# Kernel optimization log

Hardware: AMD Instinct MI355X
Metric: run time of the kernel (lower is better)

Reference implementation:

```python
import jax, jax.numpy as jnp
import numpy as np

D_MODEL = 1024
N_HEAD = 16
D_HEAD = 64
BSZ = 2
QLEN = 2048
LOCAL_SIZE = 1000
LN_EPS = 1e-5


def setup_inputs() -> dict:
    key = jax.random.key(0)
    ks = jax.random.split(key, 8)
    z1ss = jax.random.normal(ks[0], (BSZ, D_MODEL, QLEN), jnp.float32)
    pos_emb = jax.random.normal(ks[1], (1, D_MODEL, QLEN), jnp.float32)
    u1ss = jax.random.normal(ks[2], (BSZ, 3 * N_HEAD * D_HEAD, QLEN), jnp.float32) * 0.05
    W_qkv = jax.random.normal(ks[3], (3 * N_HEAD * D_HEAD, D_MODEL), jnp.float32) * 0.02
    W_r = jax.random.normal(ks[4], (N_HEAD * D_HEAD, D_MODEL), jnp.float32) * 0.02
    r_w_bias = jax.random.uniform(ks[5], (N_HEAD, D_HEAD), jnp.float32, -0.05, 0.05)
    r_r_bias = jax.random.uniform(ks[6], (N_HEAD, D_HEAD), jnp.float32, -0.05, 0.05)
    W_o = jax.random.normal(ks[7], (D_MODEL, N_HEAD * D_HEAD), jnp.float32) * 0.02
    b_o = jnp.zeros((D_MODEL,), jnp.float32)
    return dict(z1ss=z1ss, pos_emb=pos_emb, u1ss=u1ss, W_qkv=W_qkv, W_r=W_r,
                r_w_bias=r_w_bias, r_r_bias=r_r_bias, W_o=W_o, b_o=b_o)


def _rel_shift(x):
    # Transformer-XL relative-shift trick: pad one column on the left, reshape,
    # drop first row, reshape back. x: [b, n, qlen, klen]
    b, n, q, k = x.shape
    xp = jnp.pad(x, ((0, 0), (0, 0), (0, 0), (1, 0)))
    return xp.reshape(b, n, k + 1, q)[:, :, 1:, :].reshape(b, n, q, k)


def reference(z1ss, pos_emb, u1ss, W_qkv, W_r, r_w_bias, r_r_bias, W_o, b_o):
    bsz, d_model, qlen = z1ss.shape
    n_head, d_head = r_w_bias.shape
    klen = qlen  # mems=None -> mlen=0
    scale = 1.0 / (d_head ** 0.5)

    # Conv1d(kernel_size=1, bias=False) == per-position linear
    w_heads = jnp.einsum('od,bdq->boq', W_qkv, z1ss) + u1ss        # [b, 3*n*d, q]
    r_head_k = jnp.einsum('od,dq->oq', W_r, pos_emb[0]).reshape(n_head, d_head, klen)

    q_h, k_h, v_h = jnp.split(w_heads, 3, axis=1)
    q_h = q_h.reshape(bsz, n_head, d_head, qlen)
    k_h = k_h.reshape(bsz, n_head, d_head, klen)
    v_h = v_h.reshape(bsz, n_head, d_head, klen)

    AC = jnp.einsum('bndi,bndj->bnij', q_h + r_w_bias[:, :, None], k_h)
    BD = _rel_shift(jnp.einsum('bndi,ndj->bnij', q_h + r_r_bias[:, :, None], r_head_k))
    attn_score = (AC + BD) * scale                                  # [b, n, q, k]

    # causal + local-window mask (mlen=0)
    ones = jnp.ones((qlen, klen), dtype=bool)
    mask = jnp.triu(ones, 1) | jnp.tril(ones, -LOCAL_SIZE)
    attn_score = jnp.where(mask[None, None], -jnp.inf, attn_score)

    attn_prob = jax.nn.softmax(attn_score, axis=-1)
    attn_vec = jnp.einsum('bnij,bndj->bndi', attn_prob, v_h)
    attn_vec = attn_vec.reshape(bsz, n_head * d_head, qlen)

    attn_out = jnp.einsum('od,bdq->boq', W_o, attn_vec) + b_o[None, :, None]

    # post-LN residual: layer_norm over d_model (no affine params)
    x = (attn_out + z1ss).transpose(0, 2, 1)                        # [b, q, d]
    mu = x.mean(-1, keepdims=True)
    var = ((x - mu) ** 2).mean(-1, keepdims=True)
    x = (x - mu) / jnp.sqrt(var + LN_EPS)
    return x.transpose(0, 2, 1)                                     # [b, d, q]
```

## Files before the change

kernel.cpp:

```cpp
#include <hip/hip_runtime.h>
#include <hip/hip_bf16.h>

#define D_MODEL 1024
#define N_HEAD 16
#define BSZ 2
#define QLEN 2048
#define LOCAL_SIZE 1000
#define QKV3 (3 * N_HEAD * 64)

typedef __hip_bfloat16 bf16;
typedef short bf16x8 __attribute__((ext_vector_type(8)));
typedef float f32x4 __attribute__((ext_vector_type(4)));

static __device__ __forceinline__ float b2f(bf16 x) { return __bfloat162float(x); }
static __device__ __forceinline__ float bits2f(unsigned short u) {
    return __uint_as_float(((unsigned int)u) << 16);
}
static __device__ __forceinline__ unsigned short f2bs(float x) {
    __hip_bfloat16 h = __float2bfloat16(x);
    return *(unsigned short*)&h;
}

static __device__ __forceinline__ int rmode(int m, int fl) { return (m == 2) ? fl : m; }
static __device__ __forceinline__ float ldm(const void* p, size_t i, int isf) {
    return isf ? ((const float*)p)[i] : b2f(((const bf16*)p)[i]);
}
static __device__ __forceinline__ float4 ld4(const void* p, size_t i, int isf) {
    if (isf) return ((const float4*)p)[i >> 2];
    ushort4 u = ((const ushort4*)p)[i >> 2];
    float4 f;
    f.x = bits2f(u.x); f.y = bits2f(u.y); f.z = bits2f(u.z); f.w = bits2f(u.w);
    return f;
}
static __device__ __forceinline__ ushort4 cvt4(float4 f) {
    ushort4 u;
    u.x = f2bs(f.x); u.y = f2bs(f.y); u.z = f2bs(f.z); u.w = f2bs(f.w);
    return u;
}

static __device__ __forceinline__ void glds16(const bf16* g, unsigned short* l) {
    __builtin_amdgcn_global_load_lds(
        (const __attribute__((address_space(1))) void*)g,
        (__attribute__((address_space(3))) void*)l,
        16, 0, 0);
}

__global__ void detect_kernel(const unsigned short* __restrict__ w, int* __restrict__ flag)
{
    if (threadIdx.x == 0 && blockIdx.x == 0) {
        int good = 0;
        for (int i = 0; i < 256; ++i) {
            float v = bits2f(w[i]);
            if (v == v && fabsf(v) < 8.0f) ++good;
        }
        *flag = (good >= 240) ? 0 : 1;
    }
}

__global__ __launch_bounds__(256)
void convw_all(const void* __restrict__ wq, const void* __restrict__ wr,
               const void* __restrict__ wo, bf16* __restrict__ outp,
               const int* __restrict__ flag)
{
    const int fl = *flag;
    const int blk = blockIdx.x;
    const void* in; size_t segOff;
    if (blk < 1536)      { in = wq; segOff = (size_t)blk * 2048; }
    else if (blk < 2048) { in = wr; segOff = (size_t)(blk - 1536) * 2048; }
    else                 { in = wo; segOff = (size_t)(blk - 2048) * 2048; }
    const size_t ii = segOff + (size_t)threadIdx.x * 8;
    const size_t oi = (size_t)blk * 2048 + (size_t)threadIdx.x * 8;
    if (fl) {
        float4 a = ((const float4*)in)[ii / 4];
        float4 b = ((const float4*)in)[ii / 4 + 1];
        *(ushort4*)((unsigned short*)outp + oi)     = cvt4(a);
        *(ushort4*)((unsigned short*)outp + oi + 4) = cvt4(b);
    } else {
        *(uint4*)((unsigned short*)outp + oi) = ((const uint4*)in)[ii / 8];
    }
}

__global__ __launch_bounds__(256)
void tcvt_all(const void* __restrict__ z1ss, const void* __restrict__ pos,
              bf16* __restrict__ zt, bf16* __restrict__ post,
              const int* __restrict__ flag)
{
    const int fl = *flag;
    const int zb = blockIdx.z;
    const void* in = (zb < BSZ) ? z1ss : pos;
    const size_t inOff = (zb < BSZ) ? (size_t)zb * D_MODEL * QLEN : 0;
    bf16* outp = (zb < BSZ) ? zt + (size_t)zb * QLEN * D_MODEL : post;
    const int c0 = blockIdx.x * 32;
    const int r0 = blockIdx.y * 32;
    const int tx = threadIdx.x & 31, ty = threadIdx.x >> 5;
    __shared__ float T[32][33];
#pragma unroll
    for (int r = 0; r < 4; ++r) {
        int rr = r0 + ty + r * 8;
        T[ty + r * 8][tx] = ldm(in, inOff + (size_t)rr * QLEN + c0 + tx, fl);
    }
    __syncthreads();
#pragma unroll
    for (int r = 0; r < 4; ++r) {
        int cc = c0 + ty + r * 8;
        outp[(size_t)cc * D_MODEL + r0 + tx] = __float2bfloat16(T[tx][ty + r * 8]);
    }
}

__global__ __launch_bounds__(256)
void gemm_qkvr(const bf16* __restrict__ wqb, const bf16* __restrict__ wrb,
               const bf16* __restrict__ zt, const bf16* __restrict__ post,
               bf16* __restrict__ wh, bf16* __restrict__ rhk,
               const void* __restrict__ u1ss, const int* __restrict__ flag)
{
    const int fl = *flag;
    const int bz = blockIdx.z;
    const int by = blockIdx.y;
    const bool isR = by >= (QKV3 / 128);
    if (isR && bz) return;
    const int n0 = blockIdx.x * 128;
    const int m0 = (isR ? by - QKV3 / 128 : by) * 128;
    const int K = D_MODEL, N = QLEN;

    const bf16* A = isR ? wrb : wqb;
    const bf16* B = isR ? post : zt + (size_t)bz * (size_t)QLEN * D_MODEL;
    bf16* C       = isR ? rhk  : wh + (size_t)bz * (size_t)QKV3 * QLEN;
    const size_t uOff = (size_t)bz * (size_t)QKV3 * QLEN;

    const int tid = threadIdx.x;
    const int wave = tid >> 6, lane = tid & 63;
    const int quad = lane >> 4, l15 = lane & 15;
    const int wm = (wave >> 1) * 64, wn = (wave & 1) * 64;

    __shared__ __align__(16) unsigned short A_s[2][128 * 32];
    __shared__ __align__(16) unsigned short B_s[2][128 * 32];

    const int srow = wave * 32 + (lane >> 2);
    const int scol = (lane & 3) * 8;
    const bf16* Ag = A + (size_t)(m0 + srow) * K + scol;
    const bf16* Bg = B + (size_t)(n0 + srow) * K + scol;
    const int sbase = wave * 1024;

    f32x4 acc[4][4];
#pragma unroll
    for (int i = 0; i < 4; ++i)
#pragma unroll
        for (int j = 0; j < 4; ++j) acc[i][j] = (f32x4){0.f, 0.f, 0.f, 0.f};

    glds16(Ag,                   &A_s[0][sbase]);
    glds16(Ag + (size_t)16 * K,  &A_s[0][sbase + 512]);
    glds16(Bg,                   &B_s[0][sbase]);
    glds16(Bg + (size_t)16 * K,  &B_s[0][sbase + 512]);

    int cur = 0;
    for (int k0 = 0; k0 < K; k0 += 32) {
        __syncthreads();
        if (k0 + 32 < K) {
            const int kn = k0 + 32;
            glds16(Ag + kn,                  &A_s[cur ^ 1][sbase]);
            glds16(Ag + (size_t)16 * K + kn, &A_s[cur ^ 1][sbase + 512]);
            glds16(Bg + kn,                  &B_s[cur ^ 1][sbase]);
            glds16(Bg + (size_t)16 * K + kn, &B_s[cur ^ 1][sbase + 512]);
        }
        bf16x8 a[4], bb[4];
#pragma unroll
        for (int i = 0; i < 4; ++i)
            a[i] = *(const bf16x8*)&A_s[cur][(wm + i * 16 + l15) * 32 + quad * 8];
#pragma unroll
        for (int j = 0; j < 4; ++j)
            bb[j] = *(const bf16x8*)&B_s[cur][(wn + j * 16 + l15) * 32 + quad * 8];
#pragma unroll
        for (int i = 0; i < 4; ++i)
#pragma unroll
            for (int j = 0; j < 4; ++j)
                acc[i][j] = __builtin_amdgcn_mfma_f32_16x16x32_bf16(a[i], bb[j], acc[i][j], 0, 0, 0);
        cur ^= 1;
    }

#pragma unroll
    for (int i = 0; i < 4; ++i) {
#pragma unroll
        for (int j = 0; j < 4; ++j) {
            int n = n0 + wn + j * 16 + l15;
#pragma unroll
            for (int r = 0; r < 4; ++r) {
                int m = m0 + wm + i * 16 + quad * 4 + r;
                float v = acc[i][j][r];
                if (!isR) v += ldm(u1ss, uOff + (size_t)m * N + n, fl);
                C[(size_t)m * N + n] = __float2bfloat16(v);
            }
        }
    }
}

__global__ __launch_bounds__(256)
void gemm_glds(const bf16* __restrict__ A, size_t sAb,
               const bf16* __restrict__ B, size_t sBb,
               void* __restrict__ C, int c_is_bf16, size_t sCb,
               const void* __restrict__ addm, int mAdd, size_t sAddb,
               const void* __restrict__ bias, int mBias,
               int M, int N, int K, const int* __restrict__ flag)
{
    const int fl = *flag;
    const int fAdd = rmode(mAdd, fl), fBias = rmode(mBias, fl);

    const int bz = blockIdx.z;
    const int n0 = blockIdx.x * 128;
    const int m0 = blockIdx.y * 128;
    const int tid = threadIdx.x;
    const int wave = tid >> 6, lane = tid & 63;
    const int quad = lane >> 4, l15 = lane & 15;
    const int wm = (wave >> 1) * 64, wn = (wave & 1) * 64;

    __shared__ __align__(16) unsigned short A_s[2][128 * 32];
    __shared__ __align__(16) unsigned short B_s[2][128 * 32];

    const int srow = wave * 32 + (lane >> 2);
    const int scol = (lane & 3) * 8;
    const bf16* Ag = A + (size_t)bz * sAb + (size_t)(m0 + srow) * K + scol;
    const bf16* Bg = B + (size_t)bz * sBb + (size_t)(n0 + srow) * K + scol;
    const int sbase = wave * 1024;

    f32x4 acc[4][4];
#pragma unroll
    for (int i = 0; i < 4; ++i)
#pragma unroll
        for (int j = 0; j < 4; ++j) acc[i][j] = (f32x4){0.f, 0.f, 0.f, 0.f};

    glds16(Ag,                   &A_s[0][sbase]);
    glds16(Ag + (size_t)16 * K,  &A_s[0][sbase + 512]);
    glds16(Bg,                   &B_s[0][sbase]);
    glds16(Bg + (size_t)16 * K,  &B_s[0][sbase + 512]);

    int cur = 0;
    for (int k0 = 0; k0 < K; k0 += 32) {
        __syncthreads();
        if (k0 + 32 < K) {
            const int kn = k0 + 32;
            glds16(Ag + kn,                  &A_s[cur ^ 1][sbase]);
            glds16(Ag + (size_t)16 * K + kn, &A_s[cur ^ 1][sbase + 512]);
            glds16(Bg + kn,                  &B_s[cur ^ 1][sbase]);
            glds16(Bg + (size_t)16 * K + kn, &B_s[cur ^ 1][sbase + 512]);
        }
        bf16x8 a[4], bb[4];
#pragma unroll
        for (int i = 0; i < 4; ++i)
            a[i] = *(const bf16x8*)&A_s[cur][(wm + i * 16 + l15) * 32 + quad * 8];
#pragma unroll
        for (int j = 0; j < 4; ++j)
            bb[j] = *(const bf16x8*)&B_s[cur][(wn + j * 16 + l15) * 32 + quad * 8];
#pragma unroll
        for (int i = 0; i < 4; ++i)
#pragma unroll
            for (int j = 0; j < 4; ++j)
                acc[i][j] = __builtin_amdgcn_mfma_f32_16x16x32_bf16(a[i], bb[j], acc[i][j], 0, 0, 0);
        cur ^= 1;
    }

    const size_t cb = (size_t)bz * sCb;
#pragma unroll
    for (int i = 0; i < 4; ++i) {
#pragma unroll
        for (int j = 0; j < 4; ++j) {
            int n = n0 + wn + j * 16 + l15;
#pragma unroll
            for (int r = 0; r < 4; ++r) {
                int m = m0 + wm + i * 16 + quad * 4 + r;
                float v = acc[i][j][r];
                if (addm) v += ldm(addm, (size_t)bz * sAddb + (size_t)m * N + n, fAdd);
                if (bias) v += ldm(bias, (size_t)n, fBias);
                size_t ci = cb + (size_t)m * N + n;
                if (c_is_bf16) ((bf16*)C)[ci] = __float2bfloat16(v);
                else           ((float*)C)[ci] = v;
            }
        }
    }
}

__global__ __launch_bounds__(256)
void gemm_bf16(const void* __restrict__ A, int mA, size_t sAb,
               const void* __restrict__ B, int mB, size_t sBb,
               void* __restrict__ C, int c_is_bf16, size_t sCb,
               const void* __restrict__ addm, int mAdd, size_t sAddb,
               const void* __restrict__ bias, int mBias,
               int M, int N, int K, const int* __restrict__ flag)
{
    const int fl = *flag;
    const int fA = rmode(mA, fl), fB = rmode(mB, fl);
    const int fAdd = rmode(mAdd, fl), fBias = rmode(mBias, fl);

    const int bz = blockIdx.z;
    const int n0 = blockIdx.x * 128;
    const int m0 = blockIdx.y * 128;
    const int tid = threadIdx.x;
    const int wave = tid >> 6, lane = tid & 63;
    const int quad = lane >> 4, l15 = lane & 15;
    const int wm = (wave >> 1) * 64, wn = (wave & 1) * 64;

    __shared__ unsigned short A_s[128][40];
    __shared__ unsigned short B_s[128][40];

    const int r0c = tid >> 2,         c0c = tid & 3;
    const int r1c = (tid + 256) >> 2, c1c = tid & 3;

    const size_t aOff = (size_t)bz * sAb;
    const size_t bOff = (size_t)bz * sBb;
    const bf16*  Ah = (const bf16*)A;
    const float* Af = (const float*)A;
    const bf16*  Bh = (const bf16*)B;
    const float* Bf = (const float*)B;

    uint4 pa[4], pb[4];

#define LOAD_OP(p, fX, Xh, Xf, xOff, R0, C0, R1, C1, base, k0)                          \
    do {                                                                                \
        if (!fX) {                                                                      \
            p[0] = *(const uint4*)(Xh + xOff + (size_t)(base + R0) * K + (k0) + C0 * 8);\
            p[1] = *(const uint4*)(Xh + xOff + (size_t)(base + R1) * K + (k0) + C1 * 8);\
        } else {                                                                        \
            const float* q0 = Xf + xOff + (size_t)(base + R0) * K + (k0) + C0 * 8;      \
            const float* q1 = Xf + xOff + (size_t)(base + R1) * K + (k0) + C1 * 8;      \
            p[0] = *(const uint4*)q0; p[1] = *(const uint4*)(q0 + 4);                   \
            p[2] = *(const uint4*)q1; p[3] = *(const uint4*)(q1 + 4);                   \
        }                                                                               \
    } while (0)

#define WRITE_OP(p, fX, S, R0, C0, R1, C1)                                              \
    do {                                                                                \
        if (!fX) {                                                                      \
            *(uint4*)&S[R0][C0 * 8] = p[0];                                             \
            *(uint4*)&S[R1][C1 * 8] = p[1];                                             \
        } else {                                                                        \
            float4 f0 = *(float4*)&p[0], f1 = *(float4*)&p[1];                          \
            float4 f2 = *(float4*)&p[2], f3 = *(float4*)&p[3];                          \
            *(ushort4*)&S[R0][C0 * 8]     = cvt4(f0);                                   \
            *(ushort4*)&S[R0][C0 * 8 + 4] = cvt4(f1);                                   \
            *(ushort4*)&S[R1][C1 * 8]     = cvt4(f2);                                   \
            *(ushort4*)&S[R1][C1 * 8 + 4] = cvt4(f3);                                   \
        }                                                                               \
    } while (0)

    f32x4 acc[4][4];
#pragma unroll
    for (int i = 0; i < 4; ++i)
#pragma unroll
        for (int j = 0; j < 4; ++j) acc[i][j] = (f32x4){0.f, 0.f, 0.f, 0.f};

    LOAD_OP(pa, fA, Ah, Af, aOff, r0c, c0c, r1c, c1c, m0, 0);
    LOAD_OP(pb, fB, Bh, Bf, bOff, r0c, c0c, r1c, c1c, n0, 0);

    for (int k0 = 0; k0 < K; k0 += 32) {
        WRITE_OP(pa, fA, A_s, r0c, c0c, r1c, c1c);
        WRITE_OP(pb, fB, B_s, r0c, c0c, r1c, c1c);
        __syncthreads();

        const int kn = k0 + 32;
        if (kn < K) {
            LOAD_OP(pa, fA, Ah, Af, aOff, r0c, c0c, r1c, c1c, m0, kn);
            LOAD_OP(pb, fB, Bh, Bf, bOff, r0c, c0c, r1c, c1c, n0, kn);
        }

        bf16x8 a[4], bb[4];
#pragma unroll
        for (int i = 0; i < 4; ++i)
            a[i] = *(const bf16x8*)&A_s[wm + i * 16 + l15][quad * 8];
#pragma unroll
        for (int j = 0; j < 4; ++j)
            bb[j] = *(const bf16x8*)&B_s[wn + j * 16 + l15][quad * 8];
#pragma unroll
        for (int i = 0; i < 4; ++i)
#pragma unroll
            for (int j = 0; j < 4; ++j)
                acc[i][j] = __builtin_amdgcn_mfma_f32_16x16x32_bf16(a[i], bb[j], acc[i][j], 0, 0, 0);
        __syncthreads();
    }
#undef LOAD_OP
#undef WRITE_OP

    const size_t cb = (size_t)bz * sCb;
#pragma unroll
    for (int i = 0; i < 4; ++i) {
#pragma unroll
        for (int j = 0; j < 4; ++j) {
            int n = n0 + wn + j * 16 + l15;
#pragma unroll
            for (int r = 0; r < 4; ++r) {
                int m = m0 + wm + i * 16 + quad * 4 + r;
                float v = acc[i][j][r];
                if (addm) v += ldm(addm, (size_t)bz * sAddb + (size_t)m * N + n, fAdd);
                if (bias) v += ldm(bias, (size_t)n, fBias);
                size_t ci = cb + (size_t)m * N + n;
                if (c_is_bf16) ((bf16*)C)[ci] = __float2bfloat16(v);
                else           ((float*)C)[ci] = v;
            }
        }
    }
}

__global__ __launch_bounds__(256)
void gemm_tn(const void* __restrict__ A, int mA, size_t sAb,
             const void* __restrict__ Bsrc, int mB, int bTrans, int ldB, size_t sBb,
             void* __restrict__ C, int c_is_bf16, size_t sCb,
             const void* __restrict__ addm, int mAdd, int addT, size_t sAddb,
             const void* __restrict__ bias, int mBias,
             int M, int N, int K, const int* __restrict__ flag)
{
    const int fl = *flag;
    const int fA = rmode(mA, fl), fB = rmode(mB, fl);
    const int fAdd = rmode(mAdd, fl), fBias = rmode(mBias, fl);

    const int bz = blockIdx.z;
    const int n0 = blockIdx.x * 128;
    const int m0 = blockIdx.y * 128;
    const int tid = threadIdx.x;
    const int wave = tid >> 6, lane = tid & 63;
    const int quad = lane >> 4, l15 = lane & 15;
    const int wm = (wave >> 1) * 64, wn = (wave & 1) * 64;

    __shared__ unsigned short A_s[128][40];
    __shared__ unsigned short B_s[128][40];

    const size_t aBase = (size_t)bz * sAb;
    const size_t bBase = (size_t)bz * sBb;

    f32x4 acc[4][4];
#pragma unroll
    for (int i = 0; i < 4; ++i)
#pragma unroll
        for (int j = 0; j < 4; ++j) acc[i][j] = (f32x4){0.f, 0.f, 0.f, 0.f};

    for (int k0 = 0; k0 < K; k0 += 32) {
#pragma unroll
        for (int g = 0; g < 4; ++g) {
            int c = tid + g * 256;
            int m = c >> 3, kc = (c & 7) * 4;
            float4 f = ld4(A, aBase + (size_t)(m0 + m) * K + k0 + kc, fA);
            *(ushort4*)&A_s[m][kc] = cvt4(f);
        }
        if (!bTrans) {
#pragma unroll
            for (int g = 0; g < 4; ++g) {
                int c = tid + g * 256;
                int n = c >> 3, kc = (c & 7) * 4;
                float4 f = ld4(Bsrc, bBase + (size_t)(n0 + n) * ldB + k0 + kc, fB);
                *(ushort4*)&B_s[n][kc] = cvt4(f);
            }
        } else {
#pragma unroll
            for (int g = 0; g < 4; ++g) {
                int c = tid + g * 256;
                int k = c >> 5, nc = (c & 31) * 4;
                float4 f = ld4(Bsrc, bBase + (size_t)(k0 + k) * ldB + n0 + nc, fB);
                ushort4 u = cvt4(f);
                B_s[nc + 0][k] = u.x;
                B_s[nc + 1][k] = u.y;
                B_s[nc + 2][k] = u.z;
                B_s[nc + 3][k] = u.w;
            }
        }
        __syncthreads();

        bf16x8 a[4], bb[4];
#pragma unroll
        for (int i = 0; i < 4; ++i)
            a[i] = *(const bf16x8*)&A_s[wm + i * 16 + l15][quad * 8];
#pragma unroll
        for (int j = 0; j < 4; ++j)
            bb[j] = *(const bf16x8*)&B_s[wn + j * 16 + l15][quad * 8];
#pragma unroll
        for (int i = 0; i < 4; ++i)
#pragma unroll
            for (int j = 0; j < 4; ++j)
                acc[i][j] = __builtin_amdgcn_mfma_f32_16x16x32_bf16(a[i], bb[j], acc[i][j], 0, 0, 0);
        __syncthreads();
    }

    const size_t cb = (size_t)bz * sCb;
#pragma unroll
    for (int i = 0; i < 4; ++i) {
#pragma unroll
        for (int j = 0; j < 4; ++j) {
            int n = n0 + wn + j * 16 + l15;
#pragma unroll
            for (int r = 0; r < 4; ++r) {
                int m = m0 + wm + i * 16 + quad * 4 + r;
                float v = acc[i][j][r];
                if (addm) {
                    size_t ai = (size_t)bz * sAddb +
                                (addT ? ((size_t)n * M + m) : ((size_t)m * N + n));
                    v += ldm(addm, ai, fAdd);
                }
                if (bias) v += ldm(bias, (size_t)n, fBias);
                size_t ci = cb + (size_t)m * N + n;
                if (c_is_bf16) ((bf16*)C)[ci] = __float2bfloat16(v);
                else           ((float*)C)[ci] = v;
            }
        }
    }
}

__global__ __launch_bounds__(256)
void attn_mfma(const bf16* __restrict__ wh,
               const bf16* __restrict__ rhk,
               const void* __restrict__ rwb,
               const void* __restrict__ rrb,
               bf16* __restrict__ av_out,
               const int* __restrict__ flag)
{
    const int fl = *flag;
    const int it = blockIdx.x, h = blockIdx.y, b = blockIdx.z;
    const int i0 = it * 64;
    const int tid = threadIdx.x;
    const int wave = tid >> 6, lane = tid & 63;
    const int quad = lane >> 4, l15 = lane & 15;
    const int hw = h * 64;

    __shared__ __align__(16) unsigned short sm[18944];
    unsigned short* KtPs = sm;
    unsigned short* Vs   = sm + 4608;
    unsigned short* Rt   = sm + 9216;
    unsigned short* Gs   = sm + 9216;
    unsigned short* Qrw  = sm;
    unsigned short* Qrr  = sm + 4608;

    const bf16* whb = wh + (size_t)b * QKV3 * QLEN;
    const int d_t = tid & 63;
    const int dv0 = tid >> 3, jv0 = (tid & 7) * 8;
    const int dv1 = (tid + 256) >> 3;

    int lo = i0 - (LOCAL_SIZE - 1);
    if (lo < 0) lo = 0;
    const int jt_lo = lo >> 6;
    const int j0_lo = jt_lo * 64;

    {
        float brw = ldm(rwb, hw + d_t, fl);
        float brr = ldm(rrb, hw + d_t, fl);
        const bf16* qrow = whb + (size_t)(hw + d_t) * QLEN + i0;
        uint4 qv0 = *(const uint4*)(qrow + wave * 8);
        uint4 qv1 = *(const uint4*)(qrow + (4 + wave) * 8);
        const int pbase0 = j0_lo - i0 + QLEN - 64;
        const bf16* rrow = rhk + (size_t)(hw + d_t) * QLEN;
        uint4 rv0i = *(const uint4*)(rrow + pbase0 + wave * 8);
        uint4 rv1i = *(const uint4*)(rrow + pbase0 + (4 + wave) * 8);

        unsigned short u8[8];
        *(uint4*)u8 = qv0;
#pragma unroll
        for (int u = 0; u < 8; ++u) {
            float q = bits2f(u8[u]);
            Qrw[(wave * 8 + u) * 72 + d_t] = f2bs(q + brw);
            Qrr[(wave * 8 + u) * 72 + d_t] = f2bs(q + brr);
        }
        *(uint4*)u8 = qv1;
#pragma unroll
        for (int u = 0; u < 8; ++u) {
            float q = bits2f(u8[u]);
            Qrw[((4 + wave) * 8 + u) * 72 + d_t] = f2bs(q + brw);
            Qrr[((4 + wave) * 8 + u) * 72 + d_t] = f2bs(q + brr);
        }
        *(uint4*)u8 = rv0i;
#pragma unroll
        for (int u = 0; u < 8; ++u) Rt[(wave * 8 + u) * 72 + d_t] = u8[u];
        *(uint4*)u8 = rv1i;
#pragma unroll
        for (int u = 0; u < 8; ++u) Rt[((4 + wave) * 8 + u) * 72 + d_t] = u8[u];
    }

    uint4 kv0, kv1, vv0, vv1, rv0, rv1;
    {
        const int j0 = j0_lo;
        const bf16* krow = whb + (size_t)(1024 + hw + d_t) * QLEN + j0;
        kv0 = *(const uint4*)(krow + wave * 8);
        kv1 = *(const uint4*)(krow + (4 + wave) * 8);
        vv0 = *(const uint4*)(whb + (size_t)(2048 + hw + dv0) * QLEN + j0 + jv0);
        vv1 = *(const uint4*)(whb + (size_t)(2048 + hw + dv1) * QLEN + j0 + jv0);
        const int pn = j0 - i0 + QLEN;
        const bf16* rrow = rhk + (size_t)(hw + d_t) * QLEN;
        int p0 = pn + wave * 8;
        if (p0 + 7 < QLEN) rv0 = *(const uint4*)(rrow + p0);
        else {
            unsigned short u8[8];
#pragma unroll
            for (int u = 0; u < 8; ++u)
                u8[u] = (p0 + u < QLEN) ? *(const unsigned short*)(rrow + p0 + u) : 0;
            rv0 = *(uint4*)u8;
        }
        int p1 = pn + (4 + wave) * 8;
        if (p1 + 7 < QLEN) rv1 = *(const uint4*)(rrow + p1);
        else {
            unsigned short u8[8];
#pragma unroll
            for (int u = 0; u < 8; ++u)
                u8[u] = (p1 + u < QLEN) ? *(const unsigned short*)(rrow + p1 + u) : 0;
            rv1 = *(uint4*)u8;
        }
    }
    __syncthreads();

    const int qrow_off = (wave * 16 + l15) * 72 + quad * 8;
    bf16x8 qw0 = *(const bf16x8*)&Qrw[qrow_off];
    bf16x8 qw1 = *(const bf16x8*)&Qrw[qrow_off + 32];
    bf16x8 qr0 = *(const bf16x8*)&Qrr[qrow_off];
    bf16x8 qr1 = *(const bf16x8*)&Qrr[qrow_off + 32];

    f32x4 g_acc[8];
#pragma unroll
    for (int nt = 0; nt < 4; ++nt) {
        f32x4 g = (f32x4){0.f, 0.f, 0.f, 0.f};
        int ro = (nt * 16 + l15) * 72 + quad * 8;
        bf16x8 b0 = *(const bf16x8*)&Rt[ro];
        bf16x8 b1 = *(const bf16x8*)&Rt[ro + 32];
        g = __builtin_amdgcn_mfma_f32_16x16x32_bf16(qr0, b0, g, 0, 0, 0);
        g = __builtin_amdgcn_mfma_f32_16x16x32_bf16(qr1, b1, g, 0, 0, 0);
        g_acc[nt] = g;
    }

    float l_r[4] = {0.f, 0.f, 0.f, 0.f};
    f32x4 o_acc[4];
#pragma unroll
    for (int dj = 0; dj < 4; ++dj) o_acc[dj] = (f32x4){0.f, 0.f, 0.f, 0.f};

    for (int jt = jt_lo; jt <= it; ++jt) {
        const int j0 = jt * 64;
        asm volatile("" ::: "memory");
        __builtin_amdgcn_s_barrier();
        asm volatile("" ::: "memory");

        {
            unsigned short u8[8];
            *(uint4*)u8 = kv0;
#pragma unroll
            for (int u = 0; u < 8; ++u) KtPs[(wave * 8 + u) * 72 + d_t] = u8[u];
            *(uint4*)u8 = kv1;
#pragma unroll
            for (int u = 0; u < 8; ++u) KtPs[((4 + wave) * 8 + u) * 72 + d_t] = u8[u];
            *(uint4*)&Vs[dv0 * 72 + jv0] = vv0;
            *(uint4*)&Vs[dv1 * 72 + jv0] = vv1;
            *(uint4*)u8 = rv0;
#pragma unroll
            for (int u = 0; u < 8; ++u) Rt[(wave * 8 + u) * 72 + d_t] = u8[u];
            *(uint4*)u8 = rv1;
#pragma unroll
            for (int u = 0; u < 8; ++u) Rt[((4 + wave) * 8 + u) * 72 + d_t] = u8[u];
        }

        if (jt < it) {
            const int j0n = j0 + 64;
            const bf16* krow = whb + (size_t)(1024 + hw + d_t) * QLEN + j0n;
            kv0 = *(const uint4*)(krow + wave * 8);
            kv1 = *(const uint4*)(krow + (4 + wave) * 8);
            vv0 = *(const uint4*)(whb + (size_t)(2048 + hw + dv0) * QLEN + j0n + jv0);
            vv1 = *(const uint4*)(whb + (size_t)(2048 + hw + dv1) * QLEN + j0n + jv0);
            const int pn = j0n - i0 + QLEN;
            const bf16* rrow = rhk + (size_t)(hw + d_t) * QLEN;
            int p0 = pn + wave * 8;
            if (p0 + 7 < QLEN) rv0 = *(const uint4*)(rrow + p0);
            else {
                unsigned short u8[8];
#pragma unroll
                for (int u = 0; u < 8; ++u)
                    u8[u] = (p0 + u < QLEN) ? *(const unsigned short*)(rrow + p0 + u) : 0;
                rv0 = *(uint4*)u8;
            }
            int p1 = pn + (4 + wave) * 8;
            if (p1 + 7 < QLEN) rv1 = *(const uint4*)(rrow + p1);
            else {
                unsigned short u8[8];
#pragma unroll
                for (int u = 0; u < 8; ++u)
                    u8[u] = (p1 + u < QLEN) ? *(const unsigned short*)(rrow + p1 + u) : 0;
                rv1 = *(uint4*)u8;
            }
        }
        asm volatile("s_waitcnt lgkmcnt(0)" ::: "memory");
        __builtin_amdgcn_s_barrier();
        asm volatile("" ::: "memory");

        f32x4 s_acc[4];
#pragma unroll
        for (int nj = 0; nj < 4; ++nj) {
            s_acc[nj] = (f32x4){0.f, 0.f, 0.f, 0.f};
            int ko = (nj * 16 + l15) * 72 + quad * 8;
            bf16x8 b0 = *(const bf16x8*)&KtPs[ko];
            bf16x8 b1 = *(const bf16x8*)&KtPs[ko + 32];
            s_acc[nj] = __builtin_amdgcn_mfma_f32_16x16x32_bf16(qw0, b0, s_acc[nj], 0, 0, 0);
            s_acc[nj] = __builtin_amdgcn_mfma_f32_16x16x32_bf16(qw1, b1, s_acc[nj], 0, 0, 0);
        }
#pragma unroll
        for (int nt = 0; nt < 4; ++nt) {
            f32x4 g = (f32x4){0.f, 0.f, 0.f, 0.f};
            int ro = (nt * 16 + l15) * 72 + quad * 8;
            bf16x8 b0 = *(const bf16x8*)&Rt[ro];
            bf16x8 b1 = *(const bf16x8*)&Rt[ro + 32];
            g = __builtin_amdgcn_mfma_f32_16x16x32_bf16(qr0, b0, g, 0, 0, 0);
            g = __builtin_amdgcn_mfma_f32_16x16x32_bf16(qr1, b1, g, 0, 0, 0);
            g_acc[4 + nt] = g;
        }
        asm volatile("" ::: "memory");
        __builtin_amdgcn_s_barrier();
        asm volatile("" ::: "memory");

#pragma unroll
        for (int nt = 0; nt < 8; ++nt) {
            ushort4 u;
            u.x = f2bs(g_acc[nt][0]);
            u.y = f2bs(g_acc[nt][1]);
            u.z = f2bs(g_acc[nt][2]);
            u.w = f2bs(g_acc[nt][3]);
            *(ushort4*)&Gs[(nt * 16 + l15) * 76 + wave * 16 + quad * 4] = u;
        }

        float rs[4] = {0.f, 0.f, 0.f, 0.f};
#pragma unroll
        for (int nj = 0; nj < 4; ++nj) {
#pragma unroll
            for (int r = 0; r < 4; ++r) {
                int i_loc = wave * 16 + quad * 4 + r;
                int j_loc = nj * 16 + l15;
                int t = j_loc - i_loc + 63;
                float bd = bits2f(Gs[t * 76 + i_loc]);
                int diff = (i0 + i_loc) - (j0 + j_loc);
                float p = 0.f;
                if (diff >= 0 && diff < LOCAL_SIZE)
                    p = __expf((s_acc[nj][r] + bd) * 0.125f);
                KtPs[i_loc * 72 + j_loc] = f2bs(p);
                rs[r] += p;
            }
        }
#pragma unroll
        for (int r = 0; r < 4; ++r) {
            float v = rs[r];
            v += __shfl_xor(v, 1);
            v += __shfl_xor(v, 2);
            v += __shfl_xor(v, 4);
            v += __shfl_xor(v, 8);
            l_r[r] += v;
        }

        {
            int po = (wave * 16 + l15) * 72 + quad * 8;
            bf16x8 pa0 = *(const bf16x8*)&KtPs[po];
            bf16x8 pa1 = *(const bf16x8*)&KtPs[po + 32];
#pragma unroll
            for (int dj = 0; dj < 4; ++dj) {
                int vo = (dj * 16 + l15) * 72 + quad * 8;
                bf16x8 b0 = *(const bf16x8*)&Vs[vo];
                bf16x8 b1 = *(const bf16x8*)&Vs[vo + 32];
                o_acc[dj] = __builtin_amdgcn_mfma_f32_16x16x32_bf16(pa0, b0, o_acc[dj], 0, 0, 0);
                o_acc[dj] = __builtin_amdgcn_mfma_f32_16x16x32_bf16(pa1, b1, o_acc[dj], 0, 0, 0);
            }
        }

#pragma unroll
        for (int nt = 0; nt < 4; ++nt) g_acc[nt] = g_acc[nt + 4];
    }

#pragma unroll
    for (int r = 0; r < 4; ++r) {
        float inv = 1.f / l_r[r];
        int q = i0 + wave * 16 + quad * 4 + r;
        bf16* orow = av_out + ((size_t)b * QLEN + q) * D_MODEL + hw;
#pragma unroll
        for (int dj = 0; dj < 4; ++dj)
            orow[dj * 16 + l15] = __float2bfloat16(o_acc[dj][r] * inv);
    }
}

__global__ __launch_bounds__(256)
void ln_kernel(float* __restrict__ yt)
{
    const int b = blockIdx.y, q = blockIdx.x;
    float* row = yt + ((size_t)b * QLEN + q) * D_MODEL;
    const int t = threadIdx.x;
    float4 v = ((float4*)row)[t];
    float s  = v.x + v.y + v.z + v.w;
    float ss = v.x * v.x + v.y * v.y + v.z * v.z + v.w * v.w;
#pragma unroll
    for (int off = 32; off; off >>= 1) {
        s  += __shfl_down(s, off);
        ss += __shfl_down(ss, off);
    }
    __shared__ float sw[4], ssw[4];
    const int w = t >> 6;
    if ((t & 63) == 0) { sw[w] = s; ssw[w] = ss; }
    __syncthreads();
    float S  = sw[0] + sw[1] + sw[2] + sw[3];
    float SS = ssw[0] + ssw[1] + ssw[2] + ssw[3];
    float mu  = S / D_MODEL;
    float var = SS / D_MODEL - mu * mu;
    float rs  = rsqrtf(var + 1e-5f);
    v.x = (v.x - mu) * rs; v.y = (v.y - mu) * rs;
    v.z = (v.z - mu) * rs; v.w = (v.w - mu) * rs;
    ((float4*)row)[t] = v;
}

__global__ __launch_bounds__(256)
void transpose_out(const float* __restrict__ yt, void* __restrict__ out,
                   const int* __restrict__ flag)
{
    const int fl = *flag;
    const int b  = blockIdx.z;
    const int q0 = blockIdx.x * 32;
    const int o0 = blockIdx.y * 32;
    const int tx = threadIdx.x & 31, ty = threadIdx.x >> 5;
    __shared__ float T[32][33];
#pragma unroll
    for (int r = 0; r < 4; ++r) {
        int q = q0 + ty + r * 8;
        T[ty + r * 8][tx] = yt[((size_t)b * QLEN + q) * D_MODEL + o0 + tx];
    }
    __syncthreads();
#pragma unroll
    for (int r = 0; r < 4; ++r) {
        int o = o0 + ty + r * 8;
        size_t oi = ((size_t)b * D_MODEL + o) * QLEN + q0 + tx;
        float v = T[tx][ty + r * 8];
        if (fl) ((float*)out)[oi] = v;
        else    ((bf16*)out)[oi] = __float2bfloat16(v);
    }
}

extern "C" void kernel_launch(void* const* d_in, const int* in_sizes, int n_in,
                              void* d_out, int out_size, void* d_ws, size_t ws_size,
                              hipStream_t stream)
{
    const void* z1ss = d_in[0];
    const void* pos  = d_in[1];
    const void* u1ss = d_in[2];
    const void* Wqkv = d_in[3];
    const void* Wr   = d_in[4];
    const void* rwb  = d_in[5];
    const void* rrb  = d_in[6];
    const void* Wo   = d_in[7];
    const void* bo   = d_in[8];

    const size_t whE  = (size_t)BSZ * QKV3 * QLEN;
    const size_t rhkE = (size_t)D_MODEL * QLEN;
    const size_t avE  = (size_t)BSZ * QLEN * D_MODEL;
    const size_t ztE  = avE;
    const size_t wqE  = (size_t)QKV3 * D_MODEL;
    const size_t wrE  = (size_t)D_MODEL * D_MODEL;
    const size_t woE  = wrE;

    char* ws = (char*)d_ws;
    bf16* wh   = (bf16*)ws;
    bf16* rhk  = wh + whE;
    bf16* avec = rhk + rhkE;
    bf16* post = avec;
    size_t baseB = (whE + rhkE + avE) * sizeof(bf16);
    bf16* zt  = (bf16*)(ws + baseB);
    bf16* wqb = zt + ztE;
    bf16* wrb = wqb + wqE;
    bf16* wob = wrb + wrE;
    float* yt = (float*)ws;

    const size_t t2B = baseB + ztE * sizeof(bf16) + 16;
    const size_t t1B = baseB + (ztE + wqE + wrE + woE) * sizeof(bf16) + 16;
    const int tier = (ws_size >= t1B) ? 1 : (ws_size >= t2B) ? 2 : 3;

    int* flag = (tier == 1) ? (int*)(wob + woE)
              : (tier == 2) ? (int*)(wqb)
                            : (int*)(ws + baseB);

    detect_kernel<<<1, 64, 0, stream>>>((const unsigned short*)Wqkv, flag);

    if (tier == 1) {
        convw_all<<<dim3((unsigned)((wqE + wrE + woE) / 2048)), 256, 0, stream>>>(
            Wqkv, Wr, Wo, wqb, flag);

        tcvt_all<<<dim3(QLEN / 32, D_MODEL / 32, BSZ + 1), 256, 0, stream>>>(
            z1ss, pos, zt, post, flag);

        gemm_qkvr<<<dim3(QLEN / 128, QKV3 / 128 + D_MODEL / 128, BSZ), 256, 0, stream>>>(
            wqb, wrb, zt, post, wh, rhk, u1ss, flag);

        attn_mfma<<<dim3(QLEN / 64, N_HEAD, BSZ), 256, 0, stream>>>(
            wh, rhk, rwb, rrb, avec, flag);

        gemm_glds<<<dim3(1024 / 128, 2048 / 128, BSZ), 256, 0, stream>>>(
            avec, (size_t)QLEN * D_MODEL,
            wob, 0,
            yt, 0, (size_t)QLEN * D_MODEL,
            zt, 0, (size_t)QLEN * D_MODEL,
            bo, 2,
            QLEN, D_MODEL, D_MODEL, flag);
    } else if (tier == 2) {
        tcvt_all<<<dim3(QLEN / 32, D_MODEL / 32, BSZ + 1), 256, 0, stream>>>(
            z1ss, pos, zt, post, flag);

        gemm_bf16<<<dim3(2048 / 128, 3072 / 128, BSZ), 256, 0, stream>>>(
            Wqkv, 2, 0,
            zt, 0, (size_t)QLEN * D_MODEL,
            wh, 1, (size_t)QKV3 * QLEN,
            u1ss, 2, (size_t)QKV3 * QLEN,
            nullptr, 0,
            QKV3, QLEN, D_MODEL, flag);

        gemm_bf16<<<dim3(2048 / 128, 1024 / 128, 1), 256, 0, stream>>>(
            Wr, 2, 0,
            post, 0, 0,
            rhk, 1, 0,
            nullptr, 0, 0,
            nullptr, 0,
            D_MODEL, QLEN, D_MODEL, flag);

        attn_mfma<<<dim3(QLEN / 64, N_HEAD, BSZ), 256, 0, stream>>>(
            wh, rhk, rwb, rrb, avec, flag);

        gemm_bf16<<<dim3(1024 / 128, 2048 / 128, BSZ), 256, 0, stream>>>(
            avec, 0, (size_t)QLEN * D_MODEL,
            Wo, 2, 0,
            yt, 0, (size_t)QLEN * D_MODEL,
            zt, 0, (size_t)QLEN * D_MODEL,
            bo, 2,
            QLEN, D_MODEL, D_MODEL, flag);
    } else {
        gemm_tn<<<dim3(2048 / 128, 3072 / 128, BSZ), 256, 0, stream>>>(
            Wqkv, 2, 0,
            z1ss, 2, 1, QLEN, (size_t)D_MODEL * QLEN,
            wh, 1, (size_t)QKV3 * QLEN,
            u1ss, 2, 0, (size_t)QKV3 * QLEN,
            nullptr, 0,
            QKV3, QLEN, D_MODEL, flag);
        gemm_tn<<<dim3(2048 / 128, 1024 / 128, 1), 256, 0, stream>>>(
            Wr, 2, 0,
            pos, 2, 1, QLEN, 0,
            rhk, 1, 0,
            nullptr, 0, 0, 0,
            nullptr, 0,
            D_MODEL, QLEN, D_MODEL, flag);
        attn_mfma<<<dim3(QLEN / 64, N_HEAD, BSZ), 256, 0, stream>>>(
            wh, rhk, rwb, rrb, avec, flag);
        gemm_tn<<<dim3(1024 / 128, 2048 / 128, BSZ), 256, 0, stream>>>(
            avec, 0, (size_t)QLEN * D_MODEL,
            Wo, 2, 0, D_MODEL, 0,
            yt, 0, (size_t)QLEN * D_MODEL,
            z1ss, 2, 1, (size_t)D_MODEL * QLEN,
            bo, 2,
            QLEN, D_MODEL, D_MODEL, flag);
    }

    ln_kernel<<<dim3(QLEN, BSZ), 256, 0, stream>>>(yt);

    transpose_out<<<dim3(QLEN / 32, D_MODEL / 32, BSZ), 256, 0, stream>>>(yt, d_out, flag);
}
```

Before: 413.3 us.

## Replace LDS rel-shift staging with ds_bpermute and remap blocks for load balance

The BD rel-shift values are now taken straight from other lanes' g_acc registers with ds_bpermute, instead of being written to a shared Gs buffer and read back. This removes one barrier and the LDS round-trip per key tile. P gets its own LDS region so it no longer aliases K. Block indices are also remapped so that long and short causal query tiles are interleaved across slots, to balance work. The per-wave softmax is specialised with a macro, which costs more code size and registers.

```diff
diff --git a/kernel.cpp b/kernel.cpp
--- a/kernel.cpp
+++ b/kernel.cpp
@@ -508,20 +508,28 @@
                const int* __restrict__ flag)
 {
     const int fl = *flag;
-    const int it = blockIdx.x, h = blockIdx.y, b = blockIdx.z;
+    const int lidx = blockIdx.x + 32 * (blockIdx.y + (blockIdx.z << 4));
+    const int slot = lidx >> 8;
+    const int grp  = lidx & 255;
+    const int hb   = grp & 31;
+    const int prm  = grp >> 5;
+    const int it   = (slot == 0) ? 16 + prm : (slot == 1) ? 24 + prm
+                   : (slot == 2) ? prm : 15 - prm;
+    const int h = hb & 15, b = hb >> 4;
+
     const int i0 = it * 64;
     const int tid = threadIdx.x;
     const int wave = tid >> 6, lane = tid & 63;
     const int quad = lane >> 4, l15 = lane & 15;
     const int hw = h * 64;
 
-    __shared__ __align__(16) unsigned short sm[18944];
-    unsigned short* KtPs = sm;
-    unsigned short* Vs   = sm + 4608;
-    unsigned short* Rt   = sm + 9216;
-    unsigned short* Gs   = sm + 9216;
-    unsigned short* Qrw  = sm;
-    unsigned short* Qrr  = sm + 4608;
+    __shared__ __align__(16) unsigned short sm[18432];
+    unsigned short* Kt  = sm;
+    unsigned short* Vs  = sm + 4608;
+    unsigned short* Rt  = sm + 9216;
+    unsigned short* Ps  = sm + 13824;
+    unsigned short* Qrw = sm;
+    unsigned short* Qrr = sm + 4608;
 
     const bf16* whb = wh + (size_t)b * QKV3 * QLEN;
     const int d_t = tid & 63;
@@ -631,10 +639,10 @@
             unsigned short u8[8];
             *(uint4*)u8 = kv0;
 #pragma unroll
-            for (int u = 0; u < 8; ++u) KtPs[(wave * 8 + u) * 72 + d_t] = u8[u];
+            for (int u = 0; u < 8; ++u) Kt[(wave * 8 + u) * 72 + d_t] = u8[u];
             *(uint4*)u8 = kv1;
 #pragma unroll
-            for (int u = 0; u < 8; ++u) KtPs[((4 + wave) * 8 + u) * 72 + d_t] = u8[u];
+            for (int u = 0; u < 8; ++u) Kt[((4 + wave) * 8 + u) * 72 + d_t] = u8[u];
             *(uint4*)&Vs[dv0 * 72 + jv0] = vv0;
             *(uint4*)&Vs[dv1 * 72 + jv0] = vv1;
             *(uint4*)u8 = rv0;
@@ -682,8 +690,8 @@
         for (int nj = 0; nj < 4; ++nj) {
             s_acc[nj] = (f32x4){0.f, 0.f, 0.f, 0.f};
             int ko = (nj * 16 + l15) * 72 + quad * 8;
-            bf16x8 b0 = *(const bf16x8*)&KtPs[ko];
-            bf16x8 b1 = *(const bf16x8*)&KtPs[ko + 32];
+            bf16x8 b0 = *(const bf16x8*)&Kt[ko];
+            bf16x8 b1 = *(const bf16x8*)&Kt[ko + 32];
             s_acc[nj] = __builtin_amdgcn_mfma_f32_16x16x32_bf16(qw0, b0, s_acc[nj], 0, 0, 0);
             s_acc[nj] = __builtin_amdgcn_mfma_f32_16x16x32_bf16(qw1, b1, s_acc[nj], 0, 0, 0);
         }
@@ -697,37 +705,38 @@
             g = __builtin_amdgcn_mfma_f32_16x16x32_bf16(qr1, b1, g, 0, 0, 0);
             g_acc[4 + nt] = g;
         }
-        asm volatile("" ::: "memory");
-        __builtin_amdgcn_s_barrier();
-        asm volatile("" ::: "memory");
-
-#pragma unroll
-        for (int nt = 0; nt < 8; ++nt) {
-            ushort4 u;
-            u.x = f2bs(g_acc[nt][0]);
-            u.y = f2bs(g_acc[nt][1]);
-            u.z = f2bs(g_acc[nt][2]);
-            u.w = f2bs(g_acc[nt][3]);
-            *(ushort4*)&Gs[(nt * 16 + l15) * 76 + wave * 16 + quad * 4] = u;
-        }
 
         float rs[4] = {0.f, 0.f, 0.f, 0.f};
-#pragma unroll
-        for (int nj = 0; nj < 4; ++nj) {
-#pragma unroll
-            for (int r = 0; r < 4; ++r) {
-                int i_loc = wave * 16 + quad * 4 + r;
-                int j_loc = nj * 16 + l15;
-                int t = j_loc - i_loc + 63;
-                float bd = bits2f(Gs[t * 76 + i_loc]);
-                int diff = (i0 + i_loc) - (j0 + j_loc);
-                float p = 0.f;
-                if (diff >= 0 && diff < LOCAL_SIZE)
-                    p = __expf((s_acc[nj][r] + bd) * 0.125f);
-                KtPs[i_loc * 72 + j_loc] = f2bs(p);
-                rs[r] += p;
-            }
-        }
+#define SOFTMAX_W(W)                                                            \
+        {                                                                       \
+            _Pragma("unroll")                                                   \
+            for (int nj = 0; nj < 4; ++nj) {                                    \
+                _Pragma("unroll")                                               \
+                for (int r = 0; r < 4; ++r) {                                   \
+                    const int n0 = 3 - (W) + nj;                                \
+                    int sa = ((lane & 48) | ((l15 - 4 * quad - r - 1) & 15)) << 2; \
+                    float blo = __int_as_float(__builtin_amdgcn_ds_bpermute(    \
+                        sa, __float_as_int(g_acc[n0][r])));                     \
+                    float bhi = __int_as_float(__builtin_amdgcn_ds_bpermute(    \
+                        sa, __float_as_int(g_acc[n0 + 1][r])));                 \
+                    float bd = (l15 > 4 * quad + r) ? bhi : blo;                \
+                    int i_loc = (W) * 16 + quad * 4 + r;                        \
+                    int j_loc = nj * 16 + l15;                                  \
+                    int diff = (i0 + i_loc) - (j0 + j_loc);                     \
+                    float pv = 0.f;                                             \
+                    if (diff >= 0 && diff < LOCAL_SIZE)                         \
+                        pv = __expf((s_acc[nj][r] + bd) * 0.125f);              \
+                    Ps[i_loc * 72 + j_loc] = f2bs(pv);                          \
+                    rs[r] += pv;                                                \
+                }                                                               \
+            }                                                                   \
+        }
+        if      (wave == 0) SOFTMAX_W(0)
+        else if (wave == 1) SOFTMAX_W(1)
+        else if (wave == 2) SOFTMAX_W(2)
+        else                SOFTMAX_W(3)
+#undef SOFTMAX_W
+
 #pragma unroll
         for (int r = 0; r < 4; ++r) {
             float v = rs[r];
@@ -740,8 +749,8 @@
 
         {
             int po = (wave * 16 + l15) * 72 + quad * 8;
-            bf16x8 pa0 = *(const bf16x8*)&KtPs[po];
-            bf16x8 pa1 = *(const bf16x8*)&KtPs[po + 32];
+            bf16x8 pa0 = *(const bf16x8*)&Ps[po];
+            bf16x8 pa1 = *(const bf16x8*)&Ps[po + 32];
 #pragma unroll
             for (int dj = 0; dj < 4; ++dj) {
                 int vo = (dj * 16 + l15) * 72 + quad * 8;
```

After: 405.9 us. No clear change (-1.8%).
